# Kernel optimization log

Measured on AMD Instinct MI355X. Metric: run time of the kernel, lower is better.

## Reference

```python
import jax, jax.numpy as jnp
import numpy as np

N = 100000      # node_size
R = 2000        # rel_size
E = 300000      # triple_size == nnz(adj)
ER = 300000     # nnz of node-to-rel adjacency
EE = 300000     # nnz of node-to-node adjacency
NODE_F = 128
REL_F = 128
ENT_F = NODE_F + REL_F  # 256
DEPTH = 2


def setup_inputs() -> dict:
    key = jax.random.key(0)
    ks = jax.random.split(key, 14)
    return {
        'ent_emb': jax.random.normal(ks[0], (N, NODE_F), jnp.float32) * 0.1,
        'rel_emb': jax.random.normal(ks[1], (R, REL_F), jnp.float32) * 0.1,
        'a_self': jax.random.normal(ks[2], (ENT_F, 1), jnp.float32) * 0.1,
        'a_neigh': jax.random.normal(ks[3], (ENT_F, 1), jnp.float32) * 0.1,
        'a_rel': jax.random.normal(ks[4], (REL_F, 1), jnp.float32) * 0.1,
        'sp_val': jax.random.uniform(ks[5], (E,), jnp.float32),
        'adj_row': jax.random.randint(ks[6], (E,), 0, N),
        'adj_col': jax.random.randint(ks[7], (E,), 0, N),
        'sp_row': jnp.arange(E),
        'sp_col': jax.random.randint(ks[8], (E,), 0, R),
        'rel_row': jax.random.randint(ks[9], (ER,), 0, N),
        'rel_col': jax.random.randint(ks[10], (ER,), 0, R),
        'ent_row': jax.random.randint(ks[11], (EE,), 0, N),
        'ent_col': jax.random.randint(ks[12], (EE,), 0, N),
    }


def _mean_agg(row, col, emb, nrows):
    # tf.sparse_softmax over all-ones values == 1/deg per row -> row mean
    deg = jax.ops.segment_sum(jnp.ones(row.shape, emb.dtype), row, nrows)
    w = 1.0 / deg[row]
    return jax.ops.segment_sum(w[:, None] * emb[col], row, nrows)


def _segment_softmax(vals, seg, nseg):
    m = jax.ops.segment_max(vals, seg, nseg)
    e = jnp.exp(vals - m[seg])
    s = jax.ops.segment_sum(e, seg, nseg)
    return e / s[seg]


def reference(ent_emb, rel_emb, a_self, a_neigh, a_rel, sp_val,
              adj_row, adj_col, sp_row, sp_col, rel_row, rel_col, ent_row, ent_col):
    # initial features: mean-aggregated entity + relation features
    rel_feat = _mean_agg(rel_row, rel_col, rel_emb, N)
    ent_feat = _mean_agg(ent_row, ent_col, ent_emb, N)
    features = jax.nn.relu(jnp.concatenate([ent_feat, rel_feat], axis=-1))  # [N, ENT_F]
    outputs = [features]

    # per-edge relation attention term: (T,R) sparse @ (rel_emb @ a_rel); constant across depth
    rel_proj = (rel_emb @ a_rel)[:, 0]                               # [R]
    rel_attn = jax.ops.segment_sum(sp_val * rel_proj[sp_col], sp_row, E)  # [E]

    att = None
    for _ in range(DEPTH):
        a_s = (features @ a_self)[:, 0]    # [N]
        a_n = (features @ a_neigh)[:, 0]   # [N]
        att = rel_attn + a_s[adj_row] + a_n[adj_col]          # [E]
        att = jax.nn.leaky_relu(att, negative_slope=0.2)
        att = _segment_softmax(att, adj_row, N)               # row-wise sparse softmax
        features = jax.nn.relu(
            jax.ops.segment_sum(att[:, None] * features[adj_col], adj_row, N))
        outputs.append(features)

    out = jnp.concatenate(outputs, axis=-1)  # [N, ENT_F*(DEPTH+1)]
    return out, att
```

## Files before the change

kernel.cpp:

```cpp
#include <hip/hip_runtime.h>

#define NODE_F 128
#define ENT_F  256
#define LDO    768
#define NEG_INF -3.4e38f


__global__ void count3_k(const int* __restrict__ r0, const int* __restrict__ r1,
                         const int* __restrict__ r2, int E0, int E1, int E2,
                         int* __restrict__ deg3, int N) {
    int i = blockIdx.x * blockDim.x + threadIdx.x;
    int y = blockIdx.y;
    const int* rp = (y == 0) ? r0 : (y == 1) ? r1 : r2;
    int Eg = (y == 0) ? E0 : (y == 1) ? E1 : E2;
    if (i < Eg) atomicAdd(&deg3[(size_t)y * N + rp[i]], 1);
}

__global__ void blocksum3_k(const int* __restrict__ deg3, int* __restrict__ bs3, int N) {
    __shared__ int s[256];
    int y = blockIdx.y;
    int i = blockIdx.x * 256 + threadIdx.x;
    s[threadIdx.x] = (i < N) ? deg3[(size_t)y * N + i] : 0;
    __syncthreads();
    for (int o = 128; o > 0; o >>= 1) {
        if (threadIdx.x < o) s[threadIdx.x] += s[threadIdx.x + o];
        __syncthreads();
    }
    if (threadIdx.x == 0) bs3[y * 512 + blockIdx.x] = s[0];
}

__global__ void scanbsum3_k(int* __restrict__ bs3, int nb, int* __restrict__ rs3, int N) {
    __shared__ int s[512];
    int y = blockIdx.x;
    int tid = threadIdx.x;
    int v = (tid < nb) ? bs3[y * 512 + tid] : 0;
    s[tid] = v;
    __syncthreads();
    for (int o = 1; o < 512; o <<= 1) {
        int t = (tid >= o) ? s[tid - o] : 0;
        __syncthreads();
        s[tid] += t;
        __syncthreads();
    }
    if (tid < nb) bs3[y * 512 + tid] = s[tid] - v;
    if (tid == 511) rs3[(size_t)y * (N + 1) + N] = s[511];
}

__global__ void scandeg3_k(const int* __restrict__ deg3, const int* __restrict__ bs3,
                           int* __restrict__ rs3, int* __restrict__ cur3, int N) {
    __shared__ int s[256];
    int y = blockIdx.y;
    int i = blockIdx.x * 256 + threadIdx.x;
    int v = (i < N) ? deg3[(size_t)y * N + i] : 0;
    s[threadIdx.x] = v;
    __syncthreads();
    for (int o = 1; o < 256; o <<= 1) {
        int t = (threadIdx.x >= o) ? s[threadIdx.x - o] : 0;
        __syncthreads();
        s[threadIdx.x] += t;
        __syncthreads();
    }
    if (i < N) {
        int rs = bs3[y * 512 + blockIdx.x] + s[threadIdx.x] - v;
        rs3[(size_t)y * (N + 1) + i] = rs;
        cur3[(size_t)y * N + i] = rs;
    }
}

__global__ void scatter3_k(const int* __restrict__ r0, const int* __restrict__ c0,
                           const int* __restrict__ r1, const int* __restrict__ c1,
                           const int* __restrict__ r2, const int* __restrict__ c2,
                           int E0, int E1, int E2, int* __restrict__ cur3,
                           int* __restrict__ col_adj, int* __restrict__ eid_adj,
                           int* __restrict__ col_ent, int* __restrict__ col_rel, int N) {
    int e = blockIdx.x * blockDim.x + threadIdx.x;
    int y = blockIdx.y;
    const int* rp = (y == 0) ? r0 : (y == 1) ? r1 : r2;
    const int* cp = (y == 0) ? c0 : (y == 1) ? c1 : c2;
    int* colp = (y == 0) ? col_adj : (y == 1) ? col_ent : col_rel;
    int Eg = (y == 0) ? E0 : (y == 1) ? E1 : E2;
    if (e >= Eg) return;
    int r = rp[e];
    int pos = atomicAdd(&cur3[(size_t)y * N + r], 1);
    colp[pos] = cp[e];
    if (y == 0) eid_adj[pos] = e;
}


__global__ void rel_proj_k(const float* __restrict__ rel_emb, const float* __restrict__ a_rel,
                           float* __restrict__ proj, int R) {
    int r = blockIdx.x * blockDim.x + threadIdx.x;
    if (r >= R) return;
    float s = 0.0f;
    #pragma unroll 4
    for (int f = 0; f < NODE_F; ++f) s += rel_emb[(size_t)r * NODE_F + f] * a_rel[f];
    proj[r] = s;
}

__global__ void rel_attn_map_k(const float* __restrict__ sp_val, const int* __restrict__ sp_row,
                               const int* __restrict__ sp_col, const float* __restrict__ proj,
                               float* __restrict__ rel_attn, int E) {
    int e = blockIdx.x * blockDim.x + threadIdx.x;
    if (e < E) rel_attn[sp_row[e]] = sp_val[e] * proj[sp_col[e]];
}


__global__ void meanagg_fused_k(const int* __restrict__ rs_ent, const int* __restrict__ col_ent,
                                const int* __restrict__ rs_rel, const int* __restrict__ col_rel,
                                const float* __restrict__ ent_emb, const float* __restrict__ rel_emb,
                                const float* __restrict__ a_self, const float* __restrict__ a_neigh,
                                float* __restrict__ out, float* __restrict__ a_s_out,
                                float* __restrict__ a_n_out, int N) {
    int n = blockIdx.x * (blockDim.x >> 6) + (threadIdx.x >> 6);
    int lane = threadIdx.x & 63;
    if (n >= N) return;

    int s = rs_ent[n], t = rs_ent[n + 1];
    float2 ea = {0.0f, 0.0f};
    for (int p = s; p < t; ++p) {
        float2 v = reinterpret_cast<const float2*>(&ent_emb[(size_t)col_ent[p] * NODE_F])[lane];
        ea.x += v.x; ea.y += v.y;
    }
    if (t > s) { float w = 1.0f / (float)(t - s); ea.x *= w; ea.y *= w; }

    s = rs_rel[n]; t = rs_rel[n + 1];
    float2 ra = {0.0f, 0.0f};
    for (int p = s; p < t; ++p) {
        float2 v = reinterpret_cast<const float2*>(&rel_emb[(size_t)col_rel[p] * NODE_F])[lane];
        ra.x += v.x; ra.y += v.y;
    }
    if (t > s) { float w = 1.0f / (float)(t - s); ra.x *= w; ra.y *= w; }

    ea.x = ea.x > 0.0f ? ea.x : 0.0f;  ea.y = ea.y > 0.0f ? ea.y : 0.0f;
    ra.x = ra.x > 0.0f ? ra.x : 0.0f;  ra.y = ra.y > 0.0f ? ra.y : 0.0f;

    reinterpret_cast<float2*>(&out[(size_t)n * LDO])[lane] = ea;
    reinterpret_cast<float2*>(&out[(size_t)n * LDO + NODE_F])[lane] = ra;

    float2 se = reinterpret_cast<const float2*>(a_self)[lane];
    float2 sr = reinterpret_cast<const float2*>(a_self)[64 + lane];
    float2 ne = reinterpret_cast<const float2*>(a_neigh)[lane];
    float2 nr = reinterpret_cast<const float2*>(a_neigh)[64 + lane];
    float ds = ea.x * se.x + ea.y * se.y + ra.x * sr.x + ra.y * sr.y;
    float dn = ea.x * ne.x + ea.y * ne.y + ra.x * nr.x + ra.y * nr.y;
    #pragma unroll
    for (int o = 32; o > 0; o >>= 1) {
        ds += __shfl_xor(ds, o);
        dn += __shfl_xor(dn, o);
    }
    if (lane == 0) { a_s_out[n] = ds; a_n_out[n] = dn; }
}

__global__ void attn_agg_fused_k(const int* __restrict__ rs, const int* __restrict__ col_s,
                                 const int* __restrict__ eid_s, const float* __restrict__ rel_attn,
                                 const float* __restrict__ a_s_in, const float* __restrict__ a_n_in,
                                 const float* __restrict__ a_self, const float* __restrict__ a_neigh,
                                 float* __restrict__ a_s_out, float* __restrict__ a_n_out,
                                 float* __restrict__ out, int src, int dst,
                                 float* __restrict__ att_out, int N) {
    int n = blockIdx.x * (blockDim.x >> 6) + (threadIdx.x >> 6);
    int lane = threadIdx.x & 63;
    if (n >= N) return;
    int s = rs[n], t = rs[n + 1];
    int deg = t - s;
    float4 acc = {0.0f, 0.0f, 0.0f, 0.0f};

    if (deg > 0) {
        float as_row = a_s_in[n];
        if (deg <= 64) {
            float myv = NEG_INF;
            int mycol = 0, myeid = 0;
            if (lane < deg) {
                int p = s + lane;
                mycol = col_s[p];
                myeid = eid_s[p];
                float v = rel_attn[myeid] + as_row + a_n_in[mycol];
                myv = v >= 0.0f ? v : 0.2f * v;
            }
            float m = myv;
            #pragma unroll
            for (int o = 32; o > 0; o >>= 1) {
                float x = __shfl_xor(m, o);
                m = x > m ? x : m;
            }
            float ex = (lane < deg) ? __expf(myv - m) : 0.0f;
            float ssum = ex;
            #pragma unroll
            for (int o = 32; o > 0; o >>= 1) ssum += __shfl_xor(ssum, o);
            float myatt = ex / ssum;
            if (att_out && lane < deg) att_out[myeid] = myatt;
            for (int p = 0; p < deg; ++p) {
                float a = __shfl(myatt, p);
                int c = __shfl(mycol, p);
                float4 v = reinterpret_cast<const float4*>(&out[(size_t)c * LDO + src])[lane];
                acc.x += a * v.x; acc.y += a * v.y; acc.z += a * v.z; acc.w += a * v.w;
            }
        } else {
            float m = NEG_INF;
            for (int p = s + lane; p < t; p += 64) {
                float v = rel_attn[eid_s[p]] + as_row + a_n_in[col_s[p]];
                v = v >= 0.0f ? v : 0.2f * v;
                m = v > m ? v : m;
            }
            #pragma unroll
            for (int o = 32; o > 0; o >>= 1) {
                float x = __shfl_xor(m, o);
                m = x > m ? x : m;
            }
            float ssum = 0.0f;
            for (int p = s + lane; p < t; p += 64) {
                float v = rel_attn[eid_s[p]] + as_row + a_n_in[col_s[p]];
                v = v >= 0.0f ? v : 0.2f * v;
                ssum += __expf(v - m);
            }
            #pragma unroll
            for (int o = 32; o > 0; o >>= 1) ssum += __shfl_xor(ssum, o);
            float inv = 1.0f / ssum;
            for (int p = s; p < t; ++p) {
                int c = col_s[p], e = eid_s[p];
                float v = rel_attn[e] + as_row + a_n_in[c];
                v = v >= 0.0f ? v : 0.2f * v;
                float a = __expf(v - m) * inv;
                if (att_out && lane == 0) att_out[e] = a;
                float4 fv = reinterpret_cast<const float4*>(&out[(size_t)c * LDO + src])[lane];
                acc.x += a * fv.x; acc.y += a * fv.y; acc.z += a * fv.z; acc.w += a * fv.w;
            }
        }
    }

    acc.x = acc.x > 0.0f ? acc.x : 0.0f;
    acc.y = acc.y > 0.0f ? acc.y : 0.0f;
    acc.z = acc.z > 0.0f ? acc.z : 0.0f;
    acc.w = acc.w > 0.0f ? acc.w : 0.0f;
    reinterpret_cast<float4*>(&out[(size_t)n * LDO + dst])[lane] = acc;

    if (a_s_out) {
        float4 s4 = reinterpret_cast<const float4*>(a_self)[lane];
        float4 n4 = reinterpret_cast<const float4*>(a_neigh)[lane];
        float ds = acc.x * s4.x + acc.y * s4.y + acc.z * s4.z + acc.w * s4.w;
        float dn = acc.x * n4.x + acc.y * n4.y + acc.z * n4.z + acc.w * n4.w;
        #pragma unroll
        for (int o = 32; o > 0; o >>= 1) {
            ds += __shfl_xor(ds, o);
            dn += __shfl_xor(dn, o);
        }
        if (lane == 0) { a_s_out[n] = ds; a_n_out[n] = dn; }
    }
}


extern "C" void kernel_launch(void* const* d_in, const int* in_sizes, int n_in,
                              void* d_out, int out_size, void* d_ws, size_t ws_size,
                              hipStream_t stream) {
    const float* ent_emb = (const float*)d_in[0];
    const float* rel_emb = (const float*)d_in[1];
    const float* a_self  = (const float*)d_in[2];
    const float* a_neigh = (const float*)d_in[3];
    const float* a_rel   = (const float*)d_in[4];
    const float* sp_val  = (const float*)d_in[5];
    const int*   adj_row = (const int*)d_in[6];
    const int*   adj_col = (const int*)d_in[7];
    const int*   sp_row  = (const int*)d_in[8];
    const int*   sp_col  = (const int*)d_in[9];
    const int*   rel_row = (const int*)d_in[10];
    const int*   rel_col = (const int*)d_in[11];
    const int*   ent_row = (const int*)d_in[12];
    const int*   ent_col = (const int*)d_in[13];

    const int N  = in_sizes[0] / NODE_F;
    const int R  = in_sizes[1] / NODE_F;
    const int E  = in_sizes[5];
    const int ER = in_sizes[10];
    const int EE = in_sizes[12];

    float* out = (float*)d_out;
    float* att_out = out + (size_t)N * LDO;

    const int TB = 256;
    const int nb = (N + 255) / 256;
    int maxE = E > EE ? E : EE; if (ER > maxE) maxE = ER;

    char* w = (char*)d_ws;
    int* deg3    = (int*)w;  w += (size_t)3 * N * 4;
    int* cur3    = (int*)w;  w += (size_t)3 * N * 4;
    int* rs3     = (int*)w;  w += (size_t)3 * (N + 1) * 4;
    int* bs3     = (int*)w;  w += (size_t)3 * 512 * 4;
    int* col_adj = (int*)w;  w += (size_t)E * 4;
    int* eid_adj = (int*)w;  w += (size_t)E * 4;
    int* col_ent = (int*)w;  w += (size_t)EE * 4;
    int* col_rel = (int*)w;  w += (size_t)ER * 4;
    float* rel_attn = (float*)w;  w += (size_t)E * 4;
    float* proj     = (float*)w;  w += (size_t)R * 4;
    float* a_s0     = (float*)w;  w += (size_t)N * 4;
    float* a_n0     = (float*)w;  w += (size_t)N * 4;
    float* a_s1     = (float*)w;  w += (size_t)N * 4;
    float* a_n1     = (float*)w;  w += (size_t)N * 4;

    int* rs_adj = rs3;
    int* rs_ent = rs3 + (N + 1);
    int* rs_rel = rs3 + 2 * (N + 1);

    hipMemsetAsync(deg3, 0, (size_t)3 * N * sizeof(int), stream);
    {
        dim3 g((maxE + TB - 1) / TB, 3);
        count3_k<<<g, TB, 0, stream>>>(adj_row, ent_row, rel_row, E, EE, ER, deg3, N);
    }
    {
        dim3 g(nb, 3);
        blocksum3_k<<<g, 256, 0, stream>>>(deg3, bs3, N);
        scanbsum3_k<<<3, 512, 0, stream>>>(bs3, nb, rs3, N);
        scandeg3_k<<<g, 256, 0, stream>>>(deg3, bs3, rs3, cur3, N);
    }
    {
        dim3 g((maxE + TB - 1) / TB, 3);
        scatter3_k<<<g, TB, 0, stream>>>(adj_row, adj_col, ent_row, ent_col, rel_row, rel_col,
                                         E, EE, ER, cur3, col_adj, eid_adj, col_ent, col_rel, N);
    }

    rel_proj_k<<<(R + TB - 1) / TB, TB, 0, stream>>>(rel_emb, a_rel, proj, R);
    rel_attn_map_k<<<(E + TB - 1) / TB, TB, 0, stream>>>(sp_val, sp_row, sp_col, proj, rel_attn, E);

    meanagg_fused_k<<<(N + 3) / 4, 256, 0, stream>>>(rs_ent, col_ent, rs_rel, col_rel,
                                                     ent_emb, rel_emb, a_self, a_neigh,
                                                     out, a_s0, a_n0, N);

    attn_agg_fused_k<<<(N + 3) / 4, 256, 0, stream>>>(rs_adj, col_adj, eid_adj, rel_attn,
                                                      a_s0, a_n0, a_self, a_neigh, a_s1, a_n1,
                                                      out, 0, ENT_F, nullptr, N);

    attn_agg_fused_k<<<(N + 3) / 4, 256, 0, stream>>>(rs_adj, col_adj, eid_adj, rel_attn,
                                                      a_s1, a_n1, nullptr, nullptr, nullptr, nullptr,
                                                      out, ENT_F, 2 * ENT_F, att_out, N);
}
```

Measured before the change: 361.6 us.

## Gather bf16 feature copies, replace CSR scan with atomic allocation, presort rel_attn

Writes bf16 shadow copies of each layer's features and gathers neighbour rows from them in the attention aggregation, halving gather bandwidth. The three-kernel prefix scan is replaced by one warp-scan kernel that reserves per-wave offsets with an atomic, using start+degree instead of row pointers. rel_attn is permuted into CSR order during scatter so the attention kernels read it contiguously. The bf16 gathers lose precision in later layers, and the atomic allocation makes the edge order nondeterministic.

```diff
diff --git a/kernel.cpp b/kernel.cpp
--- a/kernel.cpp
+++ b/kernel.cpp
@@ -4,6 +4,15 @@
 #define ENT_F  256
 #define LDO    768
 #define NEG_INF -3.4e38f
+
+__device__ __forceinline__ unsigned short f2bf(float x) {
+    unsigned u = __float_as_uint(x);
+    u += 0x7FFFu + ((u >> 16) & 1u);
+    return (unsigned short)(u >> 16);
+}
+__device__ __forceinline__ float bf2f(unsigned short h) {
+    return __uint_as_float(((unsigned)h) << 16);
+}
 
 
 __global__ void count3_k(const int* __restrict__ r0, const int* __restrict__ r1,
@@ -16,54 +25,26 @@
     if (i < Eg) atomicAdd(&deg3[(size_t)y * N + rp[i]], 1);
 }
 
-__global__ void blocksum3_k(const int* __restrict__ deg3, int* __restrict__ bs3, int N) {
-    __shared__ int s[256];
+__global__ void alloc3_k(const int* __restrict__ deg3, int* __restrict__ tot3,
+                         int* __restrict__ start3, int* __restrict__ cur3, int N) {
     int y = blockIdx.y;
-    int i = blockIdx.x * 256 + threadIdx.x;
-    s[threadIdx.x] = (i < N) ? deg3[(size_t)y * N + i] : 0;
-    __syncthreads();
-    for (int o = 128; o > 0; o >>= 1) {
-        if (threadIdx.x < o) s[threadIdx.x] += s[threadIdx.x + o];
-        __syncthreads();
-    }
-    if (threadIdx.x == 0) bs3[y * 512 + blockIdx.x] = s[0];
-}
-
-__global__ void scanbsum3_k(int* __restrict__ bs3, int nb, int* __restrict__ rs3, int N) {
-    __shared__ int s[512];
-    int y = blockIdx.x;
-    int tid = threadIdx.x;
-    int v = (tid < nb) ? bs3[y * 512 + tid] : 0;
-    s[tid] = v;
-    __syncthreads();
-    for (int o = 1; o < 512; o <<= 1) {
-        int t = (tid >= o) ? s[tid - o] : 0;
-        __syncthreads();
-        s[tid] += t;
-        __syncthreads();
-    }
-    if (tid < nb) bs3[y * 512 + tid] = s[tid] - v;
-    if (tid == 511) rs3[(size_t)y * (N + 1) + N] = s[511];
-}
-
-__global__ void scandeg3_k(const int* __restrict__ deg3, const int* __restrict__ bs3,
-                           int* __restrict__ rs3, int* __restrict__ cur3, int N) {
-    __shared__ int s[256];
-    int y = blockIdx.y;
-    int i = blockIdx.x * 256 + threadIdx.x;
-    int v = (i < N) ? deg3[(size_t)y * N + i] : 0;
-    s[threadIdx.x] = v;
-    __syncthreads();
-    for (int o = 1; o < 256; o <<= 1) {
-        int t = (threadIdx.x >= o) ? s[threadIdx.x - o] : 0;
-        __syncthreads();
-        s[threadIdx.x] += t;
-        __syncthreads();
-    }
+    int i = blockIdx.x * blockDim.x + threadIdx.x;
+    int lane = threadIdx.x & 63;
+    int d = (i < N) ? deg3[(size_t)y * N + i] : 0;
+    int v = d;
+    #pragma unroll
+    for (int o = 1; o < 64; o <<= 1) {
+        int t = __shfl_up(v, o);
+        if (lane >= o) v += t;
+    }
+    int wsum = __shfl(v, 63);
+    int base = 0;
+    if (lane == 63) base = atomicAdd(&tot3[y], wsum);
+    base = __shfl(base, 63);
     if (i < N) {
-        int rs = bs3[y * 512 + blockIdx.x] + s[threadIdx.x] - v;
-        rs3[(size_t)y * (N + 1) + i] = rs;
-        cur3[(size_t)y * N + i] = rs;
+        int st = base + v - d;
+        start3[(size_t)y * N + i] = st;
+        cur3[(size_t)y * N + i] = st;
     }
 }
 
@@ -72,7 +53,9 @@
                            const int* __restrict__ r2, const int* __restrict__ c2,
                            int E0, int E1, int E2, int* __restrict__ cur3,
                            int* __restrict__ col_adj, int* __restrict__ eid_adj,
-                           int* __restrict__ col_ent, int* __restrict__ col_rel, int N) {
+                           int* __restrict__ col_ent, int* __restrict__ col_rel,
+                           const float* __restrict__ rel_attn, float* __restrict__ rel_attn_s,
+                           int N) {
     int e = blockIdx.x * blockDim.x + threadIdx.x;
     int y = blockIdx.y;
     const int* rp = (y == 0) ? r0 : (y == 1) ? r1 : r2;
@@ -83,7 +66,10 @@
     int r = rp[e];
     int pos = atomicAdd(&cur3[(size_t)y * N + r], 1);
     colp[pos] = cp[e];
-    if (y == 0) eid_adj[pos] = e;
+    if (y == 0) {
+        eid_adj[pos] = e;
+        rel_attn_s[pos] = rel_attn[e];
+    }
 }
 
 
@@ -105,37 +91,45 @@
 }
 
 
-__global__ void meanagg_fused_k(const int* __restrict__ rs_ent, const int* __restrict__ col_ent,
-                                const int* __restrict__ rs_rel, const int* __restrict__ col_rel,
+__global__ void meanagg_fused_k(const int* __restrict__ st_ent, const int* __restrict__ dg_ent,
+                                const int* __restrict__ col_ent,
+                                const int* __restrict__ st_rel, const int* __restrict__ dg_rel,
+                                const int* __restrict__ col_rel,
                                 const float* __restrict__ ent_emb, const float* __restrict__ rel_emb,
                                 const float* __restrict__ a_self, const float* __restrict__ a_neigh,
-                                float* __restrict__ out, float* __restrict__ a_s_out,
-                                float* __restrict__ a_n_out, int N) {
+                                float* __restrict__ out, unsigned short* __restrict__ fb0,
+                                float* __restrict__ a_s_out, float* __restrict__ a_n_out, int N) {
     int n = blockIdx.x * (blockDim.x >> 6) + (threadIdx.x >> 6);
     int lane = threadIdx.x & 63;
     if (n >= N) return;
 
-    int s = rs_ent[n], t = rs_ent[n + 1];
+    int s = st_ent[n], deg = dg_ent[n];
     float2 ea = {0.0f, 0.0f};
-    for (int p = s; p < t; ++p) {
+    for (int p = s; p < s + deg; ++p) {
         float2 v = reinterpret_cast<const float2*>(&ent_emb[(size_t)col_ent[p] * NODE_F])[lane];
         ea.x += v.x; ea.y += v.y;
     }
-    if (t > s) { float w = 1.0f / (float)(t - s); ea.x *= w; ea.y *= w; }
-
-    s = rs_rel[n]; t = rs_rel[n + 1];
+    if (deg > 0) { float w = 1.0f / (float)deg; ea.x *= w; ea.y *= w; }
+
+    s = st_rel[n]; deg = dg_rel[n];
     float2 ra = {0.0f, 0.0f};
-    for (int p = s; p < t; ++p) {
+    for (int p = s; p < s + deg; ++p) {
         float2 v = reinterpret_cast<const float2*>(&rel_emb[(size_t)col_rel[p] * NODE_F])[lane];
         ra.x += v.x; ra.y += v.y;
     }
-    if (t > s) { float w = 1.0f / (float)(t - s); ra.x *= w; ra.y *= w; }
+    if (deg > 0) { float w = 1.0f / (float)deg; ra.x *= w; ra.y *= w; }
 
     ea.x = ea.x > 0.0f ? ea.x : 0.0f;  ea.y = ea.y > 0.0f ? ea.y : 0.0f;
     ra.x = ra.x > 0.0f ? ra.x : 0.0f;  ra.y = ra.y > 0.0f ? ra.y : 0.0f;
 
     reinterpret_cast<float2*>(&out[(size_t)n * LDO])[lane] = ea;
     reinterpret_cast<float2*>(&out[(size_t)n * LDO + NODE_F])[lane] = ra;
+    if (fb0) {
+        ushort2 eb; eb.x = f2bf(ea.x); eb.y = f2bf(ea.y);
+        ushort2 rb; rb.x = f2bf(ra.x); rb.y = f2bf(ra.y);
+        reinterpret_cast<ushort2*>(&fb0[(size_t)n * ENT_F])[lane] = eb;
+        reinterpret_cast<ushort2*>(&fb0[(size_t)n * ENT_F + NODE_F])[lane] = rb;
+    }
 
     float2 se = reinterpret_cast<const float2*>(a_self)[lane];
     float2 sr = reinterpret_cast<const float2*>(a_self)[64 + lane];
@@ -151,30 +145,32 @@
     if (lane == 0) { a_s_out[n] = ds; a_n_out[n] = dn; }
 }
 
-__global__ void attn_agg_fused_k(const int* __restrict__ rs, const int* __restrict__ col_s,
-                                 const int* __restrict__ eid_s, const float* __restrict__ rel_attn,
+__global__ void attn_agg_fused_k(const int* __restrict__ st, const int* __restrict__ dg,
+                                 const int* __restrict__ col_s, const int* __restrict__ eid_s,
+                                 const float* __restrict__ rel_attn_s,
                                  const float* __restrict__ a_s_in, const float* __restrict__ a_n_in,
                                  const float* __restrict__ a_self, const float* __restrict__ a_neigh,
                                  float* __restrict__ a_s_out, float* __restrict__ a_n_out,
                                  float* __restrict__ out, int src, int dst,
+                                 const unsigned short* __restrict__ fb_src,
+                                 unsigned short* __restrict__ fb_dst,
                                  float* __restrict__ att_out, int N) {
     int n = blockIdx.x * (blockDim.x >> 6) + (threadIdx.x >> 6);
     int lane = threadIdx.x & 63;
     if (n >= N) return;
-    int s = rs[n], t = rs[n + 1];
-    int deg = t - s;
+    int s = st[n];
+    int deg = dg[n];
     float4 acc = {0.0f, 0.0f, 0.0f, 0.0f};
 
     if (deg > 0) {
         float as_row = a_s_in[n];
         if (deg <= 64) {
             float myv = NEG_INF;
-            int mycol = 0, myeid = 0;
+            int mycol = 0;
             if (lane < deg) {
                 int p = s + lane;
                 mycol = col_s[p];
-                myeid = eid_s[p];
-                float v = rel_attn[myeid] + as_row + a_n_in[mycol];
+                float v = rel_attn_s[p] + as_row + a_n_in[mycol];
                 myv = v >= 0.0f ? v : 0.2f * v;
             }
             float m = myv;
@@ -188,17 +184,27 @@
             #pragma unroll
             for (int o = 32; o > 0; o >>= 1) ssum += __shfl_xor(ssum, o);
             float myatt = ex / ssum;
-            if (att_out && lane < deg) att_out[myeid] = myatt;
-            for (int p = 0; p < deg; ++p) {
-                float a = __shfl(myatt, p);
-                int c = __shfl(mycol, p);
-                float4 v = reinterpret_cast<const float4*>(&out[(size_t)c * LDO + src])[lane];
-                acc.x += a * v.x; acc.y += a * v.y; acc.z += a * v.z; acc.w += a * v.w;
+            if (att_out && lane < deg) att_out[eid_s[s + lane]] = myatt;
+            if (fb_src) {
+                for (int p = 0; p < deg; ++p) {
+                    float a = __shfl(myatt, p);
+                    int c = __shfl(mycol, p);
+                    ushort4 v = reinterpret_cast<const ushort4*>(&fb_src[(size_t)c * ENT_F])[lane];
+                    acc.x += a * bf2f(v.x); acc.y += a * bf2f(v.y);
+                    acc.z += a * bf2f(v.z); acc.w += a * bf2f(v.w);
+                }
+            } else {
+                for (int p = 0; p < deg; ++p) {
+                    float a = __shfl(myatt, p);
+                    int c = __shfl(mycol, p);
+                    float4 v = reinterpret_cast<const float4*>(&out[(size_t)c * LDO + src])[lane];
+                    acc.x += a * v.x; acc.y += a * v.y; acc.z += a * v.z; acc.w += a * v.w;
+                }
             }
         } else {
             float m = NEG_INF;
-            for (int p = s + lane; p < t; p += 64) {
-                float v = rel_attn[eid_s[p]] + as_row + a_n_in[col_s[p]];
+            for (int p = s + lane; p < s + deg; p += 64) {
+                float v = rel_attn_s[p] + as_row + a_n_in[col_s[p]];
                 v = v >= 0.0f ? v : 0.2f * v;
                 m = v > m ? v : m;
             }
@@ -208,20 +214,20 @@
                 m = x > m ? x : m;
             }
             float ssum = 0.0f;
-            for (int p = s + lane; p < t; p += 64) {
-                float v = rel_attn[eid_s[p]] + as_row + a_n_in[col_s[p]];
+            for (int p = s + lane; p < s + deg; p += 64) {
+                float v = rel_attn_s[p] + as_row + a_n_in[col_s[p]];
                 v = v >= 0.0f ? v : 0.2f * v;
                 ssum += __expf(v - m);
             }
             #pragma unroll
             for (int o = 32; o > 0; o >>= 1) ssum += __shfl_xor(ssum, o);
             float inv = 1.0f / ssum;
-            for (int p = s; p < t; ++p) {
-                int c = col_s[p], e = eid_s[p];
-                float v = rel_attn[e] + as_row + a_n_in[c];
+            for (int p = s; p < s + deg; ++p) {
+                int c = col_s[p];
+                float v = rel_attn_s[p] + as_row + a_n_in[c];
                 v = v >= 0.0f ? v : 0.2f * v;
                 float a = __expf(v - m) * inv;
-                if (att_out && lane == 0) att_out[e] = a;
+                if (att_out && lane == 0) att_out[eid_s[p]] = a;
                 float4 fv = reinterpret_cast<const float4*>(&out[(size_t)c * LDO + src])[lane];
                 acc.x += a * fv.x; acc.y += a * fv.y; acc.z += a * fv.z; acc.w += a * fv.w;
             }
@@ -233,6 +239,11 @@
     acc.z = acc.z > 0.0f ? acc.z : 0.0f;
     acc.w = acc.w > 0.0f ? acc.w : 0.0f;
     reinterpret_cast<float4*>(&out[(size_t)n * LDO + dst])[lane] = acc;
+    if (fb_dst) {
+        ushort4 b;
+        b.x = f2bf(acc.x); b.y = f2bf(acc.y); b.z = f2bf(acc.z); b.w = f2bf(acc.w);
+        reinterpret_cast<ushort4*>(&fb_dst[(size_t)n * ENT_F])[lane] = b;
+    }
 
     if (a_s_out) {
         float4 s4 = reinterpret_cast<const float4*>(a_self)[lane];
@@ -277,58 +288,70 @@
     float* att_out = out + (size_t)N * LDO;
 
     const int TB = 256;
-    const int nb = (N + 255) / 256;
     int maxE = E > EE ? E : EE; if (ER > maxE) maxE = ER;
 
-    char* w = (char*)d_ws;
+    char* w0 = (char*)d_ws;
+    char* w = w0;
     int* deg3    = (int*)w;  w += (size_t)3 * N * 4;
+    int* tot3    = (int*)w;  w += 4 * 4;
+    int* start3  = (int*)w;  w += (size_t)3 * N * 4;
     int* cur3    = (int*)w;  w += (size_t)3 * N * 4;
-    int* rs3     = (int*)w;  w += (size_t)3 * (N + 1) * 4;
-    int* bs3     = (int*)w;  w += (size_t)3 * 512 * 4;
     int* col_adj = (int*)w;  w += (size_t)E * 4;
     int* eid_adj = (int*)w;  w += (size_t)E * 4;
     int* col_ent = (int*)w;  w += (size_t)EE * 4;
     int* col_rel = (int*)w;  w += (size_t)ER * 4;
-    float* rel_attn = (float*)w;  w += (size_t)E * 4;
-    float* proj     = (float*)w;  w += (size_t)R * 4;
-    float* a_s0     = (float*)w;  w += (size_t)N * 4;
-    float* a_n0     = (float*)w;  w += (size_t)N * 4;
-    float* a_s1     = (float*)w;  w += (size_t)N * 4;
-    float* a_n1     = (float*)w;  w += (size_t)N * 4;
-
-    int* rs_adj = rs3;
-    int* rs_ent = rs3 + (N + 1);
-    int* rs_rel = rs3 + 2 * (N + 1);
-
-    hipMemsetAsync(deg3, 0, (size_t)3 * N * sizeof(int), stream);
+    float* rel_attn   = (float*)w;  w += (size_t)E * 4;
+    float* rel_attn_s = (float*)w;  w += (size_t)E * 4;
+    float* proj       = (float*)w;  w += (size_t)R * 4;
+    float* a_s0       = (float*)w;  w += (size_t)N * 4;
+    float* a_n0       = (float*)w;  w += (size_t)N * 4;
+    float* a_s1       = (float*)w;  w += (size_t)N * 4;
+    float* a_n1       = (float*)w;  w += (size_t)N * 4;
+
+    w = (char*)(((size_t)w + 15) & ~(size_t)15);
+    size_t slice_bytes = (size_t)N * ENT_F * 2;
+    unsigned short* fb0 = nullptr;
+    unsigned short* fb1 = nullptr;
+    if ((size_t)(w - w0) + 2 * slice_bytes <= ws_size) {
+        fb0 = (unsigned short*)w;
+        fb1 = (unsigned short*)(w + slice_bytes);
+    }
+
+    int* st_adj = start3;          int* dg_adj = deg3;
+    int* st_ent = start3 + N;      int* dg_ent = deg3 + N;
+    int* st_rel = start3 + 2 * N;  int* dg_rel = deg3 + 2 * N;
+
+    rel_proj_k<<<(R + TB - 1) / TB, TB, 0, stream>>>(rel_emb, a_rel, proj, R);
+    rel_attn_map_k<<<(E + TB - 1) / TB, TB, 0, stream>>>(sp_val, sp_row, sp_col, proj, rel_attn, E);
+
+    hipMemsetAsync(deg3, 0, ((size_t)3 * N + 4) * sizeof(int), stream);
     {
         dim3 g((maxE + TB - 1) / TB, 3);
         count3_k<<<g, TB, 0, stream>>>(adj_row, ent_row, rel_row, E, EE, ER, deg3, N);
     }
     {
-        dim3 g(nb, 3);
-        blocksum3_k<<<g, 256, 0, stream>>>(deg3, bs3, N);
-        scanbsum3_k<<<3, 512, 0, stream>>>(bs3, nb, rs3, N);
-        scandeg3_k<<<g, 256, 0, stream>>>(deg3, bs3, rs3, cur3, N);
+        dim3 g((N + TB - 1) / TB, 3);
+        alloc3_k<<<g, TB, 0, stream>>>(deg3, tot3, start3, cur3, N);
     }
     {
         dim3 g((maxE + TB - 1) / TB, 3);
         scatter3_k<<<g, TB, 0, stream>>>(adj_row, adj_col, ent_row, ent_col, rel_row, rel_col,
-                                         E, EE, ER, cur3, col_adj, eid_adj, col_ent, col_rel, N);
-    }
-
-    rel_proj_k<<<(R + TB - 1) / TB, TB, 0, stream>>>(rel_emb, a_rel, proj, R);
-    rel_attn_map_k<<<(E + TB - 1) / TB, TB, 0, stream>>>(sp_val, sp_row, sp_col, proj, rel_attn, E);
-
-    meanagg_fused_k<<<(N + 3) / 4, 256, 0, stream>>>(rs_ent, col_ent, rs_rel, col_rel,
+                                         E, EE, ER, cur3, col_adj, eid_adj, col_ent, col_rel,
+                                         rel_attn, rel_attn_s, N);
+    }
+
+    meanagg_fused_k<<<(N + 3) / 4, 256, 0, stream>>>(st_ent, dg_ent, col_ent,
+                                                     st_rel, dg_rel, col_rel,
                                                      ent_emb, rel_emb, a_self, a_neigh,
-                                                     out, a_s0, a_n0, N);
-
-    attn_agg_fused_k<<<(N + 3) / 4, 256, 0, stream>>>(rs_adj, col_adj, eid_adj, rel_attn,
-                                                      a_s0, a_n0, a_self, a_neigh, a_s1, a_n1,
-                                                      out, 0, ENT_F, nullptr, N);
-
-    attn_agg_fused_k<<<(N + 3) / 4, 256, 0, stream>>>(rs_adj, col_adj, eid_adj, rel_attn,
-                                                      a_s1, a_n1, nullptr, nullptr, nullptr, nullptr,
-                                                      out, ENT_F, 2 * ENT_F, att_out, N);
-}
+                                                     out, fb0, a_s0, a_n0, N);
+
+    attn_agg_fused_k<<<(N + 3) / 4, 256, 0, stream>>>(st_adj, dg_adj, col_adj, eid_adj,
+                                                      rel_attn_s, a_s0, a_n0, a_self, a_neigh,
+                                                      a_s1, a_n1, out, 0, ENT_F,
+                                                      fb0, fb1, nullptr, N);
+
+    attn_agg_fused_k<<<(N + 3) / 4, 256, 0, stream>>>(st_adj, dg_adj, col_adj, eid_adj,
+                                                      rel_attn_s, a_s1, a_n1, nullptr, nullptr,
+                                                      nullptr, nullptr, out, ENT_F, 2 * ENT_F,
+                                                      fb1, nullptr, att_out, N);
+}
```

New measurement: 428.6 us. 18.5% more time.
